# Performance work log

Measured on AMD Instinct MI355X. Metric: run time of the kernel, lower is better.

## Reference

```python
import jax, jax.numpy as jnp
import numpy as np

N, E, K = 50000, 1_000_000, 512
C, HALF, L, HID, NT = 64, 32, 16, 1024, 11
EPS = 1e-5


def _bn(x, gamma, beta):
    # BatchNorm1d in training mode: biased batch stats over node axis
    m = x.mean(axis=0)
    v = x.var(axis=0)
    return gamma * (x - m) * jax.lax.rsqrt(v + EPS) + beta


def _biconv(x, src, dst, w, n):
    # adjacency @ x  ->  out_i = sum_{(j->i) in edges} x_j  (edge (src=j, dst=i))
    out = jax.ops.segment_sum(x[src], dst, num_segments=n) @ w[0]
    # adjacency_t @ x -> scatter along src
    back = jax.ops.segment_sum(x[dst], src, num_segments=n) @ w[1]
    return jnp.concatenate([out, back], axis=1)  # [n, C]


def setup_inputs() -> dict:
    key = jax.random.key(0)
    ks = jax.random.split(key, 12)
    return {
        "node_types": jax.random.randint(ks[0], (N,), 0, NT, dtype=jnp.int32),
        "edge_index": jax.random.randint(ks[1], (2, E), 0, N, dtype=jnp.int32),
        "indices": jax.random.randint(ks[2], (K,), 0, N, dtype=jnp.int32),
        "emb": jax.random.normal(ks[3], (NT, C), dtype=jnp.float32),
        "conv0_w": jax.random.normal(ks[4], (2, C, HALF), dtype=jnp.float32) * 0.18,
        "res_bn_gamma": jnp.ones((L, 2, C), dtype=jnp.float32),
        "res_bn_beta": jnp.zeros((L, 2, C), dtype=jnp.float32),
        "res_w": jax.random.normal(ks[5], (L, 2, 2, C, HALF), dtype=jnp.float32) * 0.18,
        "hidden_w": jax.random.normal(ks[6], (18 * C, HID), dtype=jnp.float32) * 0.03,
        "hidden_b": jnp.zeros((HID,), dtype=jnp.float32),
        "out_w": jax.random.normal(ks[7], (HID, 1), dtype=jnp.float32) * 0.03,
        "out_b": jnp.zeros((1,), dtype=jnp.float32),
    }


def reference(node_types, edge_index, indices, emb, conv0_w, res_bn_gamma,
              res_bn_beta, res_w, hidden_w, hidden_b, out_w, out_b):
    n = node_types.shape[0]
    src, dst = edge_index[0], edge_index[1]

    x = emb[node_types]                       # [N, C] embedding lookup
    log0 = x
    x = _biconv(x, src, dst, conv0_w, n)      # conv0
    log1 = x

    def step(x, p):
        gamma, beta, w = p                    # [2,C], [2,C], [2,2,C,HALF]
        skip = x
        h = _bn(jax.nn.relu(x), gamma[0], beta[0])
        h = _biconv(h, src, dst, w[0], n)
        h = _bn(jax.nn.relu(h), gamma[1], beta[1])
        h = _biconv(h, src, dst, w[1], n)
        x = skip + h
        return x, x

    _, ys = jax.lax.scan(step, x, (res_bn_gamma, res_bn_beta, res_w))  # ys [L,N,C]

    full = jnp.concatenate(
        [log0, log1, ys.transpose(1, 0, 2).reshape(n, L * C)], axis=1)  # [N, 18*C]
    sel = full[indices]                        # [K, 18*C]
    h = jax.nn.relu(sel) @ hidden_w + hidden_b
    o = (jax.nn.relu(h) @ out_w + out_b).squeeze(-1)  # [K]
    return jax.nn.softmax(o, axis=0)
```

## Files before the change

### kernel.cpp

```cpp
#include <hip/hip_runtime.h>
#include <hip/hip_bf16.h>

#define NN 50000
#define NE 1000000
#define CC 64
#define LL 16
#define KSEL 512
#define HIDD 1024
#define FULLW 1152
#define EPSV 1e-5f


__global__ __launch_bounds__(256) void hist_kernel(const int* __restrict__ src,
    const int* __restrict__ dst, int* __restrict__ cnt_in, int* __restrict__ cnt_out) {
  int stride = gridDim.x * blockDim.x;
  for (int e = blockIdx.x * blockDim.x + threadIdx.x; e < NE; e += stride) {
    atomicAdd(&cnt_in[dst[e]], 1);
    atomicAdd(&cnt_out[src[e]], 1);
  }
}

__global__ __launch_bounds__(1024) void scan_kernel(const int* __restrict__ cnt,
    int* __restrict__ rp) {
  const int* c = cnt + blockIdx.x * NN;
  int* r = rp + blockIdx.x * (NN + 1);
  __shared__ int part[1024];
  int t = threadIdx.x;
  const int CH = (NN + 1023) / 1024;
  int beg = t * CH;
  int end = min(beg + CH, NN);
  int s = 0;
  for (int i = beg; i < end; ++i) s += c[i];
  part[t] = s;
  __syncthreads();
  for (int off = 1; off < 1024; off <<= 1) {
    int v = (t >= off) ? part[t - off] : 0;
    __syncthreads();
    part[t] += v;
    __syncthreads();
  }
  int off0 = part[t] - s;
  for (int i = beg; i < end; ++i) { r[i] = off0; off0 += c[i]; }
  if (t == 1023) r[NN] = off0;
}

__global__ __launch_bounds__(256) void initcur_kernel(const int* __restrict__ rp_in,
    const int* __restrict__ rp_out, int* __restrict__ cur_in, int* __restrict__ cur_out,
    float* __restrict__ statsA) {
  int i = blockIdx.x * 256 + threadIdx.x;
  if (i < NN) cur_in[i] = rp_in[i];
  else if (i < 2 * NN) cur_out[i - NN] = rp_out[i - NN];
  if (blockIdx.x == 0 && threadIdx.x < 128) statsA[threadIdx.x] = 0.f;
}

__global__ __launch_bounds__(256) void fill_kernel(const int* __restrict__ src,
    const int* __restrict__ dst, int* __restrict__ cur_in, int* __restrict__ cur_out,
    int* __restrict__ col_in, int* __restrict__ col_out) {
  int stride = gridDim.x * blockDim.x;
  for (int e = blockIdx.x * blockDim.x + threadIdx.x; e < NE; e += stride) {
    int s = src[e], d = dst[e];
    int p = atomicAdd(&cur_in[d], 1);
    col_in[p] = s;
    int q = atomicAdd(&cur_out[s], 1);
    col_out[q] = d;
  }
}


__global__ __launch_bounds__(256) void embed_kernel(const int* __restrict__ nt,
    const float* __restrict__ emb, float* __restrict__ X) {
  int id = blockIdx.x * 256 + threadIdx.x;
  if (id >= NN * CC) return;
  X[id] = emb[nt[id >> 6] * CC + (id & 63)];
}

__global__ __launch_bounds__(256) void gather_sel_kernel(const float* __restrict__ xsrc,
    const int* __restrict__ idx, float* __restrict__ sel, int coloff) {
  int tid = blockIdx.x * 256 + threadIdx.x;
  if (tid >= KSEL * CC) return;
  int k = tid >> 6, cch = tid & 63;
  sel[k * FULLW + coloff + cch] = xsrc[idx[k] * CC + cch];
}


__global__ __launch_bounds__(256) void mm_kernel(const float* __restrict__ X,
    float* __restrict__ Y, const float* __restrict__ W,
    const float* __restrict__ stats, const float* __restrict__ gamma,
    const float* __restrict__ beta, float* __restrict__ stats_zero) {
  int t = threadIdx.x;
  int lane = t & 63;
  int wid = t >> 6;
  float wreg[CC];
  {
    const float* wb = W + (lane >> 5) * 2048 + (lane & 31);
#pragma unroll
    for (int c2 = 0; c2 < CC; ++c2) wreg[c2] = wb[c2 * 32];
  }
  __shared__ float sc[CC], sh[CC];
  __shared__ __align__(16) float Xs[64][CC];
  if (t < CC) {
    float scale = 1.f, shift = 0.f;
    if (stats) {
      float m = stats[t] * (1.f / NN);
      float v = stats[CC + t] * (1.f / NN) - m * m;
      float is = rsqrtf(v + EPSV);
      scale = gamma[t] * is;
      shift = beta[t] - m * scale;
    }
    sc[t] = scale; sh[t] = shift;
  }
  if (stats_zero && blockIdx.x == 0 && t < 128) stats_zero[t] = 0.f;
  const bool bn = (stats != nullptr);
  for (int row0 = blockIdx.x * 64; row0 < NN; row0 += gridDim.x * 64) {
    int nrows = min(64, NN - row0);
    __syncthreads();
    for (int idx = t; idx < nrows * 16; idx += 256) {
      int r = idx >> 4, cq = idx & 15;
      float4 v = *(const float4*)(X + (size_t)(row0 + r) * CC + cq * 4);
      if (bn) {
        int c0 = cq * 4;
        v.x = fmaxf(v.x, 0.f) * sc[c0]     + sh[c0];
        v.y = fmaxf(v.y, 0.f) * sc[c0 + 1] + sh[c0 + 1];
        v.z = fmaxf(v.z, 0.f) * sc[c0 + 2] + sh[c0 + 2];
        v.w = fmaxf(v.w, 0.f) * sc[c0 + 3] + sh[c0 + 3];
      }
      *(float4*)&Xs[r][cq * 4] = v;
    }
    __syncthreads();
    for (int r = wid; r < nrows; r += 4) {
      const float* xr = &Xs[r][0];
      float a0 = 0.f, a1 = 0.f, a2 = 0.f, a3 = 0.f;
#pragma unroll
      for (int c2 = 0; c2 < CC; c2 += 4) {
        float4 xv = *(const float4*)(xr + c2);
        a0 += xv.x * wreg[c2];
        a1 += xv.y * wreg[c2 + 1];
        a2 += xv.z * wreg[c2 + 2];
        a3 += xv.w * wreg[c2 + 3];
      }
      Y[(size_t)(row0 + r) * CC + lane] = (a0 + a1) + (a2 + a3);
    }
  }
}


__global__ __launch_bounds__(256) void seg_kernel(
    const float* __restrict__ Y, const float* skip, float* OUT,
    const int* __restrict__ rp_in, const int* __restrict__ col_in,
    const int* __restrict__ rp_out, const int* __restrict__ col_out,
    float* __restrict__ stats_acc) {
  int t = threadIdx.x;
  int w = t >> 6;
  int d = (t >> 5) & 1;
  int l31 = t & 31;
  int s = l31 >> 3;
  int cb = l31 & 7;
  const int* rp = d ? rp_out : rp_in;
  const int* col = d ? col_out : col_in;
  float s1[4], s2[4];
#pragma unroll
  for (int k = 0; k < 4; ++k) { s1[k] = 0.f; s2[k] = 0.f; }

  for (int i = blockIdx.x * 4 + w; i < NN; i += gridDim.x * 4) {
    int beg = rp[i];
    int deg = rp[i + 1] - beg;
    int idx[8];
#pragma unroll
    for (int b = 0; b < 8; ++b) {
      int e = s + b * 4;
      idx[b] = (e < deg) ? col[beg + e] : -1;
    }
    float acc0[4] = {0.f, 0.f, 0.f, 0.f};
    float acc1[4] = {0.f, 0.f, 0.f, 0.f};
#pragma unroll
    for (int b = 0; b < 8; ++b) {
      if (idx[b] >= 0) {
        float4 v = *(const float4*)(Y + (((size_t)idx[b]) << 6) + (d << 5) + (cb << 2));
        float* a = (b & 1) ? acc1 : acc0;
        a[0] += v.x; a[1] += v.y; a[2] += v.z; a[3] += v.w;
      }
    }
    for (int e = s + 32; e < deg; e += 4) {
      int j = col[beg + e];
      float4 v = *(const float4*)(Y + (((size_t)j) << 6) + (d << 5) + (cb << 2));
      acc0[0] += v.x; acc0[1] += v.y; acc0[2] += v.z; acc0[3] += v.w;
    }
    float acc[4];
#pragma unroll
    for (int k = 0; k < 4; ++k) acc[k] = acc0[k] + acc1[k];
#pragma unroll
    for (int m = 8; m <= 16; m <<= 1) {
#pragma unroll
      for (int k = 0; k < 4; ++k) acc[k] += __shfl_xor(acc[k], m, 64);
    }
    if (s == 0) {
      size_t obase = (size_t)i * CC + d * 32 + cb * 4;
      if (skip) {
        float4 k0 = *(const float4*)(skip + obase);
        acc[0] += k0.x; acc[1] += k0.y; acc[2] += k0.z; acc[3] += k0.w;
      }
      *(float4*)(OUT + obase) = make_float4(acc[0], acc[1], acc[2], acc[3]);
      if (stats_acc) {
#pragma unroll
        for (int k = 0; k < 4; ++k) {
          float r = fmaxf(acc[k], 0.f);
          s1[k] += r; s2[k] += r * r;
        }
      }
    }
  }
  if (stats_acc) {
    __shared__ float red1[256], red2[256];
    if (s == 0) {
      int q = ((w * 2 + d) * 8 + cb) * 4;
#pragma unroll
      for (int k = 0; k < 4; ++k) { red1[q + k] = s1[k]; red2[q + k] = s2[k]; }
    }
    __syncthreads();
    if (t < 64) {
      int dd = t >> 5, cc = (t >> 2) & 7, k = t & 3;
      float v1 = 0.f, v2 = 0.f;
#pragma unroll
      for (int ww = 0; ww < 4; ++ww) {
        int q = ((ww * 2 + dd) * 8 + cc) * 4 + k;
        v1 += red1[q]; v2 += red2[q];
      }
      atomicAdd(&stats_acc[t], v1);
      atomicAdd(&stats_acc[CC + t], v2);
    }
  }
}


__global__ __launch_bounds__(256) void hidden_kernel(const float* __restrict__ sel,
    const float* __restrict__ Wh, const float* __restrict__ bh, float* __restrict__ h1) {
  int t = threadIdx.x;
  int lane = t & 63, w = t >> 6;
  int jb = blockIdx.x & 15;
  int rbg = blockIdx.x >> 4;
  int j = jb * 64 + lane;
  int r0 = rbg * 16;
  __shared__ __align__(16) float Ws[64][64];
  __shared__ __align__(16) float Ss[16][64];
  float acc[4] = {0.f, 0.f, 0.f, 0.f};
  for (int k0 = 0; k0 < FULLW; k0 += 64) {
    __syncthreads();
    {
      int col = (t & 15) * 4;
      int kk = t >> 4;
#pragma unroll
      for (int p = 0; p < 4; ++p) {
        float4 v = *(const float4*)(Wh + (size_t)(k0 + kk + p * 16) * HIDD + jb * 64 + col);
        *(float4*)&Ws[kk + p * 16][col] = v;
      }
      float4 v = *(const float4*)(sel + (size_t)(r0 + kk) * FULLW + k0 + col);
      v.x = fmaxf(v.x, 0.f); v.y = fmaxf(v.y, 0.f);
      v.z = fmaxf(v.z, 0.f); v.w = fmaxf(v.w, 0.f);
      *(float4*)&Ss[kk][col] = v;
    }
    __syncthreads();
    float wreg[64];
#pragma unroll
    for (int kk = 0; kk < 64; ++kk) wreg[kk] = Ws[kk][lane];
#pragma unroll
    for (int rr = 0; rr < 4; ++rr) {
      const float4* sr = (const float4*)&Ss[w * 4 + rr][0];
      float a0 = 0.f, a1 = 0.f, a2 = 0.f, a3 = 0.f;
#pragma unroll
      for (int kq = 0; kq < 16; ++kq) {
        float4 sv = sr[kq];
        a0 += sv.x * wreg[kq * 4];
        a1 += sv.y * wreg[kq * 4 + 1];
        a2 += sv.z * wreg[kq * 4 + 2];
        a3 += sv.w * wreg[kq * 4 + 3];
      }
      acc[rr] += (a0 + a1) + (a2 + a3);
    }
  }
#pragma unroll
  for (int rr = 0; rr < 4; ++rr)
    h1[(size_t)(r0 + w * 4 + rr) * HIDD + j] = acc[rr] + bh[j];
}

__global__ __launch_bounds__(256) void out_kernel(const float* __restrict__ h1,
    const float* __restrict__ ow, const float* __restrict__ ob, float* __restrict__ logits) {
  int k = blockIdx.x * 4 + (threadIdx.x >> 6);
  int lane = threadIdx.x & 63;
  if (k >= KSEL) return;
  float a = 0.f;
  for (int j = lane; j < HIDD; j += 64) {
    float v = h1[k * HIDD + j];
    a += fmaxf(v, 0.f) * ow[j];
  }
  for (int off = 32; off; off >>= 1) a += __shfl_down(a, off, 64);
  if (lane == 0) logits[k] = a + ob[0];
}

__global__ __launch_bounds__(512) void softmax_kernel(const float* __restrict__ logits,
    float* __restrict__ out) {
  int t = threadIdx.x;
  float v = logits[t];
  __shared__ float red[512];
  red[t] = v;
  __syncthreads();
  for (int s = 256; s; s >>= 1) { if (t < s) red[t] = fmaxf(red[t], red[t + s]); __syncthreads(); }
  float mx = red[0];
  __syncthreads();
  float e = expf(v - mx);
  red[t] = e;
  __syncthreads();
  for (int s = 256; s; s >>= 1) { if (t < s) red[t] += red[t + s]; __syncthreads(); }
  out[t] = e / red[0];
}


extern "C" void kernel_launch(void* const* d_in, const int* in_sizes, int n_in,
                              void* d_out, int out_size, void* d_ws, size_t ws_size,
                              hipStream_t stream) {
  const int* node_types = (const int*)d_in[0];
  const int* edge_index = (const int*)d_in[1];
  const int* indices = (const int*)d_in[2];
  const float* emb = (const float*)d_in[3];
  const float* conv0_w = (const float*)d_in[4];
  const float* bn_g = (const float*)d_in[5];
  const float* bn_b = (const float*)d_in[6];
  const float* res_w = (const float*)d_in[7];
  const float* hw = (const float*)d_in[8];
  const float* hb = (const float*)d_in[9];
  const float* ow = (const float*)d_in[10];
  const float* ob = (const float*)d_in[11];
  float* out = (float*)d_out;
  const int* src = edge_index;
  const int* dst = edge_index + NE;

  char* p = (char*)d_ws;
  size_t off = 0;
  auto alloc = [&](size_t bytes) -> void* {
    void* q = p + off;
    off += (bytes + 255) & ~(size_t)255;
    return q;
  };
  int* cnt = (int*)alloc(2 * NN * sizeof(int));
  int* rp = (int*)alloc(2 * (NN + 1) * sizeof(int));
  int* cur = (int*)alloc(2 * NN * sizeof(int));
  int* col_in = (int*)alloc((size_t)NE * sizeof(int));
  int* col_out = (int*)alloc((size_t)NE * sizeof(int));
  float* X = (float*)alloc((size_t)NN * CC * 4);
  float* H = (float*)alloc((size_t)NN * CC * 4);
  float* Y = (float*)alloc((size_t)NN * CC * 4);
  float* statsA = (float*)alloc(128 * 4);
  float* statsB = (float*)alloc(128 * 4);
  float* sel = (float*)alloc((size_t)KSEL * FULLW * 4);
  float* h1 = (float*)alloc((size_t)KSEL * HIDD * 4);
  float* logits = (float*)alloc(KSEL * 4);
  (void)ws_size; (void)in_sizes; (void)n_in; (void)out_size;

  int* cnt_in = cnt;  int* cnt_out = cnt + NN;
  int* rp_in = rp;    int* rp_out = rp + NN + 1;
  int* cur_in = cur;  int* cur_out = cur + NN;

  hipMemsetAsync(cnt, 0, 2 * NN * sizeof(int), stream);
  hipLaunchKernelGGL(hist_kernel, dim3(1024), dim3(256), 0, stream, src, dst, cnt_in, cnt_out);
  hipLaunchKernelGGL(scan_kernel, dim3(2), dim3(1024), 0, stream, cnt, rp);
  hipLaunchKernelGGL(initcur_kernel, dim3((2 * NN + 255) / 256), dim3(256), 0, stream,
                     rp_in, rp_out, cur_in, cur_out, statsA);
  hipLaunchKernelGGL(fill_kernel, dim3(1024), dim3(256), 0, stream, src, dst,
                     cur_in, cur_out, col_in, col_out);

  hipLaunchKernelGGL(embed_kernel, dim3((NN * CC + 255) / 256), dim3(256), 0, stream,
                     node_types, emb, X);
  hipLaunchKernelGGL(gather_sel_kernel, dim3(KSEL * CC / 256), dim3(256), 0, stream,
                     X, indices, sel, 0);

  hipLaunchKernelGGL(mm_kernel, dim3(782), dim3(256), 0, stream, X, Y, conv0_w,
                     (const float*)nullptr, (const float*)nullptr, (const float*)nullptr,
                     (float*)nullptr);
  hipLaunchKernelGGL(seg_kernel, dim3(2500), dim3(256), 0, stream, Y, (const float*)nullptr, X,
                     rp_in, col_in, rp_out, col_out, statsA);
  hipLaunchKernelGGL(gather_sel_kernel, dim3(KSEL * CC / 256), dim3(256), 0, stream,
                     X, indices, sel, CC);

  for (int l = 0; l < LL; ++l) {
    const float* w1 = res_w + (size_t)(l * 2 + 0) * 4096;
    const float* w2 = res_w + (size_t)(l * 2 + 1) * 4096;
    const float* g1 = bn_g + (l * 2 + 0) * CC;
    const float* b1 = bn_b + (l * 2 + 0) * CC;
    const float* g2 = bn_g + (l * 2 + 1) * CC;
    const float* b2 = bn_b + (l * 2 + 1) * CC;
    hipLaunchKernelGGL(mm_kernel, dim3(782), dim3(256), 0, stream, X, Y, w1, statsA, g1, b1, statsB);
    hipLaunchKernelGGL(seg_kernel, dim3(2500), dim3(256), 0, stream, Y, (const float*)nullptr, H,
                       rp_in, col_in, rp_out, col_out, statsB);
    hipLaunchKernelGGL(mm_kernel, dim3(782), dim3(256), 0, stream, H, Y, w2, statsB, g2, b2, statsA);
    hipLaunchKernelGGL(seg_kernel, dim3(2500), dim3(256), 0, stream, Y, X, X,
                       rp_in, col_in, rp_out, col_out, statsA);
    hipLaunchKernelGGL(gather_sel_kernel, dim3(KSEL * CC / 256), dim3(256), 0, stream,
                       X, indices, sel, 2 * CC + l * CC);
  }

  hipLaunchKernelGGL(hidden_kernel, dim3(512), dim3(256), 0, stream, sel, hw, hb, h1);
  hipLaunchKernelGGL(out_kernel, dim3(KSEL / 4), dim3(256), 0, stream, h1, ow, ob, logits);
  hipLaunchKernelGGL(softmax_kernel, dim3(1), dim3(512), 0, stream, logits, out);
}
```

Baseline: 4.375 ms.

## Tile CSR adjacency by source range to localize gathers in cache

Builds the in/out CSR with four sub-rows per node, keyed by which 12800-row slice of the source range each neighbor falls in. The segment-sum kernel then makes four passes, each gathering only from one slice of Y, and accumulates into OUT across passes. The intent is to keep the gathered working set cache-resident and reduce random memory traffic. In exchange it adds repeated reads and writes of OUT, four times the row-pointer traffic, poorer utilization from short per-tile degrees, and a smaller grid.

```diff
diff --git a/kernel.cpp b/kernel.cpp
--- a/kernel.cpp
+++ b/kernel.cpp
@@ -9,26 +9,30 @@
 #define HIDD 1024
 #define FULLW 1152
 #define EPSV 1e-5f
+#define NTILE 4
+#define TROWS 12800
+#define RPN (4 * NN)
 
 
 __global__ __launch_bounds__(256) void hist_kernel(const int* __restrict__ src,
     const int* __restrict__ dst, int* __restrict__ cnt_in, int* __restrict__ cnt_out) {
   int stride = gridDim.x * blockDim.x;
   for (int e = blockIdx.x * blockDim.x + threadIdx.x; e < NE; e += stride) {
-    atomicAdd(&cnt_in[dst[e]], 1);
-    atomicAdd(&cnt_out[src[e]], 1);
+    int s = src[e], d = dst[e];
+    atomicAdd(&cnt_in[d * NTILE + s / TROWS], 1);
+    atomicAdd(&cnt_out[s * NTILE + d / TROWS], 1);
   }
 }
 
 __global__ __launch_bounds__(1024) void scan_kernel(const int* __restrict__ cnt,
     int* __restrict__ rp) {
-  const int* c = cnt + blockIdx.x * NN;
-  int* r = rp + blockIdx.x * (NN + 1);
+  const int* c = cnt + blockIdx.x * RPN;
+  int* r = rp + blockIdx.x * (RPN + 1);
   __shared__ int part[1024];
   int t = threadIdx.x;
-  const int CH = (NN + 1023) / 1024;
+  const int CH = (RPN + 1023) / 1024;
   int beg = t * CH;
-  int end = min(beg + CH, NN);
+  int end = min(beg + CH, RPN);
   int s = 0;
   for (int i = beg; i < end; ++i) s += c[i];
   part[t] = s;
@@ -41,15 +45,15 @@
   }
   int off0 = part[t] - s;
   for (int i = beg; i < end; ++i) { r[i] = off0; off0 += c[i]; }
-  if (t == 1023) r[NN] = off0;
+  if (t == 1023) r[RPN] = off0;
 }
 
 __global__ __launch_bounds__(256) void initcur_kernel(const int* __restrict__ rp_in,
     const int* __restrict__ rp_out, int* __restrict__ cur_in, int* __restrict__ cur_out,
     float* __restrict__ statsA) {
   int i = blockIdx.x * 256 + threadIdx.x;
-  if (i < NN) cur_in[i] = rp_in[i];
-  else if (i < 2 * NN) cur_out[i - NN] = rp_out[i - NN];
+  if (i < RPN) cur_in[i] = rp_in[i];
+  else if (i < 2 * RPN) cur_out[i - RPN] = rp_out[i - RPN];
   if (blockIdx.x == 0 && threadIdx.x < 128) statsA[threadIdx.x] = 0.f;
 }
 
@@ -59,9 +63,9 @@
   int stride = gridDim.x * blockDim.x;
   for (int e = blockIdx.x * blockDim.x + threadIdx.x; e < NE; e += stride) {
     int s = src[e], d = dst[e];
-    int p = atomicAdd(&cur_in[d], 1);
+    int p = atomicAdd(&cur_in[d * NTILE + s / TROWS], 1);
     col_in[p] = s;
-    int q = atomicAdd(&cur_out[s], 1);
+    int q = atomicAdd(&cur_out[s * NTILE + d / TROWS], 1);
     col_out[q] = d;
   }
 }
@@ -161,50 +165,60 @@
 #pragma unroll
   for (int k = 0; k < 4; ++k) { s1[k] = 0.f; s2[k] = 0.f; }
 
-  for (int i = blockIdx.x * 4 + w; i < NN; i += gridDim.x * 4) {
-    int beg = rp[i];
-    int deg = rp[i + 1] - beg;
-    int idx[8];
-#pragma unroll
-    for (int b = 0; b < 8; ++b) {
-      int e = s + b * 4;
-      idx[b] = (e < deg) ? col[beg + e] : -1;
-    }
-    float acc0[4] = {0.f, 0.f, 0.f, 0.f};
-    float acc1[4] = {0.f, 0.f, 0.f, 0.f};
-#pragma unroll
-    for (int b = 0; b < 8; ++b) {
-      if (idx[b] >= 0) {
-        float4 v = *(const float4*)(Y + (((size_t)idx[b]) << 6) + (d << 5) + (cb << 2));
-        float* a = (b & 1) ? acc1 : acc0;
-        a[0] += v.x; a[1] += v.y; a[2] += v.z; a[3] += v.w;
-      }
-    }
-    for (int e = s + 32; e < deg; e += 4) {
-      int j = col[beg + e];
-      float4 v = *(const float4*)(Y + (((size_t)j) << 6) + (d << 5) + (cb << 2));
-      acc0[0] += v.x; acc0[1] += v.y; acc0[2] += v.z; acc0[3] += v.w;
-    }
-    float acc[4];
-#pragma unroll
-    for (int k = 0; k < 4; ++k) acc[k] = acc0[k] + acc1[k];
-#pragma unroll
-    for (int m = 8; m <= 16; m <<= 1) {
-#pragma unroll
-      for (int k = 0; k < 4; ++k) acc[k] += __shfl_xor(acc[k], m, 64);
-    }
-    if (s == 0) {
-      size_t obase = (size_t)i * CC + d * 32 + cb * 4;
-      if (skip) {
-        float4 k0 = *(const float4*)(skip + obase);
-        acc[0] += k0.x; acc[1] += k0.y; acc[2] += k0.z; acc[3] += k0.w;
-      }
-      *(float4*)(OUT + obase) = make_float4(acc[0], acc[1], acc[2], acc[3]);
-      if (stats_acc) {
-#pragma unroll
-        for (int k = 0; k < 4; ++k) {
-          float r = fmaxf(acc[k], 0.f);
-          s1[k] += r; s2[k] += r * r;
+  for (int tile = 0; tile < NTILE; ++tile) {
+    const bool first = (tile == 0);
+    const bool last = (tile == NTILE - 1);
+    for (int i = blockIdx.x * 4 + w; i < NN; i += gridDim.x * 4) {
+      int rbase = (i << 2) | tile;
+      int beg = rp[rbase];
+      int deg = rp[rbase + 1] - beg;
+      int idx[8];
+#pragma unroll
+      for (int b = 0; b < 8; ++b) {
+        int e = s + b * 4;
+        idx[b] = (e < deg) ? col[beg + e] : -1;
+      }
+      float acc0[4] = {0.f, 0.f, 0.f, 0.f};
+      float acc1[4] = {0.f, 0.f, 0.f, 0.f};
+#pragma unroll
+      for (int b = 0; b < 8; ++b) {
+        if (idx[b] >= 0) {
+          float4 v = *(const float4*)(Y + (((size_t)idx[b]) << 6) + (d << 5) + (cb << 2));
+          float* a = (b & 1) ? acc1 : acc0;
+          a[0] += v.x; a[1] += v.y; a[2] += v.z; a[3] += v.w;
+        }
+      }
+      for (int e = s + 32; e < deg; e += 4) {
+        int j = col[beg + e];
+        float4 v = *(const float4*)(Y + (((size_t)j) << 6) + (d << 5) + (cb << 2));
+        acc0[0] += v.x; acc0[1] += v.y; acc0[2] += v.z; acc0[3] += v.w;
+      }
+      float acc[4];
+#pragma unroll
+      for (int k = 0; k < 4; ++k) acc[k] = acc0[k] + acc1[k];
+#pragma unroll
+      for (int m = 8; m <= 16; m <<= 1) {
+#pragma unroll
+        for (int k = 0; k < 4; ++k) acc[k] += __shfl_xor(acc[k], m, 64);
+      }
+      if (s == 0) {
+        size_t obase = (size_t)i * CC + d * 32 + cb * 4;
+        if (first) {
+          if (skip) {
+            float4 k0 = *(const float4*)(skip + obase);
+            acc[0] += k0.x; acc[1] += k0.y; acc[2] += k0.z; acc[3] += k0.w;
+          }
+        } else {
+          float4 k0 = *(const float4*)(OUT + obase);
+          acc[0] += k0.x; acc[1] += k0.y; acc[2] += k0.z; acc[3] += k0.w;
+        }
+        *(float4*)(OUT + obase) = make_float4(acc[0], acc[1], acc[2], acc[3]);
+        if (last && stats_acc) {
+#pragma unroll
+          for (int k = 0; k < 4; ++k) {
+            float r = fmaxf(acc[k], 0.f);
+            s1[k] += r; s2[k] += r * r;
+          }
         }
       }
     }
@@ -340,9 +354,9 @@
     off += (bytes + 255) & ~(size_t)255;
     return q;
   };
-  int* cnt = (int*)alloc(2 * NN * sizeof(int));
-  int* rp = (int*)alloc(2 * (NN + 1) * sizeof(int));
-  int* cur = (int*)alloc(2 * NN * sizeof(int));
+  int* cnt = (int*)alloc(2 * RPN * sizeof(int));
+  int* rp = (int*)alloc(2 * (RPN + 1) * sizeof(int));
+  int* cur = (int*)alloc(2 * RPN * sizeof(int));
   int* col_in = (int*)alloc((size_t)NE * sizeof(int));
   int* col_out = (int*)alloc((size_t)NE * sizeof(int));
   float* X = (float*)alloc((size_t)NN * CC * 4);
@@ -355,14 +369,14 @@
   float* logits = (float*)alloc(KSEL * 4);
   (void)ws_size; (void)in_sizes; (void)n_in; (void)out_size;
 
-  int* cnt_in = cnt;  int* cnt_out = cnt + NN;
-  int* rp_in = rp;    int* rp_out = rp + NN + 1;
-  int* cur_in = cur;  int* cur_out = cur + NN;
-
-  hipMemsetAsync(cnt, 0, 2 * NN * sizeof(int), stream);
+  int* cnt_in = cnt;  int* cnt_out = cnt + RPN;
+  int* rp_in = rp;    int* rp_out = rp + RPN + 1;
+  int* cur_in = cur;  int* cur_out = cur + RPN;
+
+  hipMemsetAsync(cnt, 0, 2 * RPN * sizeof(int), stream);
   hipLaunchKernelGGL(hist_kernel, dim3(1024), dim3(256), 0, stream, src, dst, cnt_in, cnt_out);
   hipLaunchKernelGGL(scan_kernel, dim3(2), dim3(1024), 0, stream, cnt, rp);
-  hipLaunchKernelGGL(initcur_kernel, dim3((2 * NN + 255) / 256), dim3(256), 0, stream,
+  hipLaunchKernelGGL(initcur_kernel, dim3((2 * RPN + 255) / 256), dim3(256), 0, stream,
                      rp_in, rp_out, cur_in, cur_out, statsA);
   hipLaunchKernelGGL(fill_kernel, dim3(1024), dim3(256), 0, stream, src, dst,
                      cur_in, cur_out, col_in, col_out);
@@ -375,7 +389,7 @@
   hipLaunchKernelGGL(mm_kernel, dim3(782), dim3(256), 0, stream, X, Y, conv0_w,
                      (const float*)nullptr, (const float*)nullptr, (const float*)nullptr,
                      (float*)nullptr);
-  hipLaunchKernelGGL(seg_kernel, dim3(2500), dim3(256), 0, stream, Y, (const float*)nullptr, X,
+  hipLaunchKernelGGL(seg_kernel, dim3(1024), dim3(256), 0, stream, Y, (const float*)nullptr, X,
                      rp_in, col_in, rp_out, col_out, statsA);
   hipLaunchKernelGGL(gather_sel_kernel, dim3(KSEL * CC / 256), dim3(256), 0, stream,
                      X, indices, sel, CC);
@@ -388,10 +402,10 @@
     const float* g2 = bn_g + (l * 2 + 1) * CC;
     const float* b2 = bn_b + (l * 2 + 1) * CC;
     hipLaunchKernelGGL(mm_kernel, dim3(782), dim3(256), 0, stream, X, Y, w1, statsA, g1, b1, statsB);
-    hipLaunchKernelGGL(seg_kernel, dim3(2500), dim3(256), 0, stream, Y, (const float*)nullptr, H,
+    hipLaunchKernelGGL(seg_kernel, dim3(1024), dim3(256), 0, stream, Y, (const float*)nullptr, H,
                        rp_in, col_in, rp_out, col_out, statsB);
     hipLaunchKernelGGL(mm_kernel, dim3(782), dim3(256), 0, stream, H, Y, w2, statsB, g2, b2, statsA);
-    hipLaunchKernelGGL(seg_kernel, dim3(2500), dim3(256), 0, stream, Y, X, X,
+    hipLaunchKernelGGL(seg_kernel, dim3(1024), dim3(256), 0, stream, Y, X, X,
                        rp_in, col_in, rp_out, col_out, statsA);
     hipLaunchKernelGGL(gather_sel_kernel, dim3(KSEL * CC / 256), dim3(256), 0, stream,
                        X, indices, sel, 2 * CC + l * CC);
```

Result: slower. 5.075 ms (+16.0%).
